# Performance work log

Hardware: AMD Instinct MI355X
Metric: run time of the kernel (lower is better)

The kernel has to match this reference:

```python
import jax, jax.numpy as jnp
import numpy as np

B, L, C, W, NH, FS = 8, 8, 64, 32, 128, 5
PAD = FS // 2
LN_EPS = 1e-5


def _conv(x, w, b, pad):
    y = jax.lax.conv_general_dilated(x, w, (1, 1), [(pad, pad), (pad, pad)],
                                     dimension_numbers=('NCHW', 'OIHW', 'NCHW'))
    return y + b[None, :, None, None]


def _stem(x, w1, b1, lnw, lnb, w2, b2):
    # conv(fs) -> LayerNorm over [C,W,W] -> ReLU -> conv(1x1)
    y = _conv(x, w1, b1, PAD)
    mu = jnp.mean(y, axis=(1, 2, 3), keepdims=True)
    var = jnp.var(y, axis=(1, 2, 3), keepdims=True)
    y = (y - mu) * jax.lax.rsqrt(var + LN_EPS) * lnw[None] + lnb[None]
    return _conv(jax.nn.relu(y), w2, b2, 0)


def setup_inputs() -> dict:
    key = jax.random.key(0)
    ks = jax.random.split(key, 8)
    f = lambda k, shp: jax.random.normal(k, shp, jnp.float32) * 0.02
    return {
        'in_query': jax.random.normal(ks[0], (B, C, W, W), jnp.float32),
        'in_keys': jax.random.normal(ks[1], (B, L, C, W, W), jnp.float32),
        'in_values': jax.random.normal(ks[2], (B, L, C, W, W), jnp.float32),
        's_w1': f(ks[3], (C, C, FS, FS)), 's_b1': jnp.zeros((C,), jnp.float32),
        's_lnw': jnp.ones((C, W, W), jnp.float32), 's_lnb': jnp.zeros((C, W, W), jnp.float32),
        's_w2': f(ks[4], (NH, C, 1, 1)), 's_b2': jnp.zeros((NH,), jnp.float32),
        'c_w1': f(ks[5], (C, C, FS, FS)), 'c_b1': jnp.zeros((C,), jnp.float32),
        'c_lnw': jnp.ones((C, W, W), jnp.float32), 'c_lnb': jnp.zeros((C, W, W), jnp.float32),
        'c_w2': f(ks[6], (NH, C, 1, 1)), 'c_b2': jnp.zeros((NH,), jnp.float32),
    }


def reference(in_query, in_keys, in_values,
              s_w1, s_b1, s_lnw, s_lnb, s_w2, s_b2,
              c_w1, c_b1, c_lnw, c_lnb, c_w2, c_b2):
    b, c, w, h = in_query.shape
    l = in_keys.shape[1]
    # ---- spatial attention: tokens = pixels, features = channels ----
    qf = in_query.reshape(b, c, w * h).transpose(0, 2, 1)            # [B, WH, C]
    kf = in_keys.transpose(0, 1, 3, 4, 2).reshape(b, l * w * h, c)   # [B, LWH, C]
    vf = in_values.transpose(0, 1, 3, 4, 2).reshape(b, l * w * h, c)
    a_sp = jax.nn.softmax(jnp.einsum('bnc,bmc->bnm', qf, kf), axis=-1)  # [B, WH, LWH]
    sp = jnp.einsum('bnm,bmc->bnc', a_sp, vf).reshape(b, w, h, c).transpose(0, 3, 1, 2)
    # ---- channel attention: tokens = channels, features = pixels ----
    qc = in_query.reshape(b, c, w * h)                               # [B, C, WH]
    kc = in_keys.reshape(b, l * c, h * w)                            # [B, LC, WH]
    vc = in_values.reshape(b, l * c, h * w)
    a_ch = jax.nn.softmax(jnp.einsum('bcn,bmn->bcm', qc, kc), axis=-1)  # [B, C, LC]
    ch = jnp.einsum('bcm,bmn->bcn', a_ch, vc).reshape(b, c, w, h)
    # ---- conv-LN-ReLU-conv stems on residual-added branches ----
    s_attn = _stem(sp + in_query, s_w1, s_b1, s_lnw, s_lnb, s_w2, s_b2)
    c_attn = _stem(ch + in_query, c_w1, c_b1, c_lnw, c_lnb, c_w2, c_b2)
    return (s_attn, c_attn)
```

## Files before the change

kernel.cpp:

```cpp
#include <hip/hip_runtime.h>


#define LOG2E 1.44269504088896340736f

typedef __attribute__((ext_vector_type(8))) short short8;
typedef __attribute__((ext_vector_type(4))) float f4;

#define MFMA16(a, b, c) __builtin_amdgcn_mfma_f32_16x16x32_bf16(a, b, c, 0, 0, 0)

#define GLOAD_LDS16(gp, lp) __builtin_amdgcn_global_load_lds( \
    (const __attribute__((address_space(1))) void*)(gp), \
    (__attribute__((address_space(3))) void*)(lp), 16, 0, 0)

__device__ __forceinline__ unsigned short f2bf(float f) {
  union { float f; unsigned u; } v; v.f = f;
  unsigned r = v.u + 0x7FFFu + ((v.u >> 16) & 1u);
  return (unsigned short)(r >> 16);
}
__device__ __forceinline__ unsigned short f2bf_rz(float f) {
  union { float f; unsigned u; } v; v.f = f;
  return (unsigned short)(v.u >> 16);
}
__device__ __forceinline__ float bf2f(unsigned short h) {
  union { unsigned u; float f; } v; v.u = ((unsigned)h) << 16;
  return v.f;
}
__device__ __forceinline__ float exp2fast(float x) {
#if __has_builtin(__builtin_amdgcn_exp2f)
  return __builtin_amdgcn_exp2f(x);
#else
  return exp2f(x);
#endif
}

#define O_STATS 0ul
#define O_W1T   256ul
#define O_W2B   409856ul
#define O_LNW   442624ul
#define O_LNB   704768ul
#define O_QT    966912ul
#define O_KSP   2015488ul
#define O_VT    10404096ul
#define O_NUM   18792704ul
#define O_DEN   35569920ul
#define O_SP    36094208ul
#define O_PCH   40288512ul
#define O_XS    40812800ul
#define O_XC    41861376ul
#define O_YT    42909952ul

__global__ __launch_bounds__(256) void k1_prep_chanS(
    const float* __restrict__ q, const float* __restrict__ keys,
    const float* __restrict__ values,
    const float* __restrict__ sw1, const float* __restrict__ slnw,
    const float* __restrict__ slnb, const float* __restrict__ sw2,
    const float* __restrict__ cw1, const float* __restrict__ clnw,
    const float* __restrict__ clnb, const float* __restrict__ cw2,
    char* __restrict__ ws)
{
  __shared__ float T[64][65];
  const int job = blockIdx.x, t = threadIdx.x;

  if (job < 2240) {
    int kind, mat = 0, sel = 0;
    if (job < 1024)      { kind = 0; mat = job >> 4; }
    else if (job < 2048) { kind = 1; mat = (job - 1024) >> 4; }
    else if (job < 2176) { kind = 2; mat = (job - 2048) >> 4; }
    else                 { kind = 3; sel = (job - 2176) >> 4; }
    const int pt = job & 15, p0 = pt * 64;
    const float* src =
        kind == 0 ? keys : kind == 1 ? values : kind == 2 ? q
        : (sel == 0 ? slnw : sel == 1 ? slnb : sel == 2 ? clnw : clnb);
    src += (size_t)mat * 65536;

    const int r0 = t >> 4, c4 = (t & 15) * 4;
    if (kind == 1) {
      unsigned short* VTp = (unsigned short*)(ws + O_VT);
      const int b = mat >> 3, l = mat & 7;
#pragma unroll
      for (int pass = 0; pass < 4; ++pass) {
        const int r = pass * 16 + r0;
        float4 v = *(const float4*)(src + (size_t)r * 1024 + p0 + c4);
        ushort4 o;
        o.x = f2bf(v.x); o.y = f2bf(v.y); o.z = f2bf(v.z); o.w = f2bf(v.w);
        *(ushort4*)(VTp + ((size_t)b * 64 + r) * 8192 + l * 1024 + p0 + c4) = o;
      }
      return;
    }
#pragma unroll
    for (int pass = 0; pass < 4; ++pass) {
      const int r = pass * 16 + r0;
      float4 v = *(const float4*)(src + (size_t)r * 1024 + p0 + c4);
      T[r][c4] = v.x; T[r][c4 + 1] = v.y; T[r][c4 + 2] = v.z; T[r][c4 + 3] = v.w;
    }
    __syncthreads();
#pragma unroll
    for (int pass = 0; pass < 2; ++pass) {
      const int p = pass * 32 + (t >> 3), cs = (t & 7) * 8;
      short8 o;
      if (kind == 0) {
#pragma unroll
        for (int j = 0; j < 8; ++j) o[j] = (short)f2bf(T[cs + j][p] * LOG2E);
        const int b = mat >> 3, l = mat & 7;
        *(short8*)((unsigned short*)(ws + O_KSP) +
                   ((size_t)b * 8192 + l * 1024 + p0 + p) * 64 + cs) = o;
      } else if (kind == 2) {
#pragma unroll
        for (int j = 0; j < 8; ++j) o[j] = (short)f2bf(T[cs + j][p]);
        *(short8*)((unsigned short*)(ws + O_QT) +
                   ((size_t)mat * 1024 + p0 + p) * 64 + cs) = o;
      } else {
#pragma unroll
        for (int j = 0; j < 8; ++j) o[j] = (short)f2bf(T[cs + j][p]);
        unsigned long off = (sel & 1) ? O_LNB : O_LNW;
        *(short8*)((unsigned short*)(ws + off) +
                   ((size_t)(sel >> 1) * 1024 + p0 + p) * 64 + cs) = o;
      }
    }
    return;
  }

  if (job < 3104) {
    unsigned i = (job - 2240) * 256u + t;
    if (i < 204800u) {
      unsigned ci = i & 63u, co = (i >> 6) & 63u, tt = i >> 12;
      unsigned off = tt % 25u, st = tt / 25u;
      const float* w = st ? cw1 : sw1;
      ((unsigned short*)(ws + O_W1T))[i] = f2bf(w[(co * 64u + ci) * 25u + off]);
      return;
    }
    i -= 204800u;
    if (i < 16384u) {
      unsigned c = i & 63u, nh = (i >> 6) & 127u, st = i >> 13;
      const float* w = st ? cw2 : sw2;
      ((unsigned short*)(ws + O_W2B))[i] = f2bf(w[nh * 64u + c]);
    }
    return;
  }

  {
    float* Sp = (float*)(ws + O_SP);
    const int bid = job - 3104;
    const int b = bid >> 5, colT = (bid >> 2) & 7, kt = bid & 3;
    const int w = t >> 6, lane = t & 63;
    const int low4 = lane & 15, quad = lane >> 4;
    const int col0 = colT * 64 + w * 16;

    f4 acc[4];
#pragma unroll
    for (int m = 0; m < 4; ++m) acc[m] = (f4){0.f, 0.f, 0.f, 0.f};

#pragma unroll
    for (int kst = 0; kst < 8; ++kst) {
      const int k = kt * 256 + kst * 32 + quad * 8;
      const float* kp = keys + ((size_t)(b * 512 + col0 + low4)) * 1024 + k;
      float4 u0 = *(const float4*)kp;
      float4 u1 = *(const float4*)(kp + 4);
      float kv[8] = {u0.x, u0.y, u0.z, u0.w, u1.x, u1.y, u1.z, u1.w};
      short8 bh, bl;
#pragma unroll
      for (int j = 0; j < 8; ++j) {
        unsigned short hi = f2bf(kv[j]);
        bh[j] = (short)hi;
        bl[j] = (short)f2bf(kv[j] - bf2f(hi));
      }
#pragma unroll
      for (int m = 0; m < 4; ++m) {
        const float* qp = q + ((size_t)(b * 64 + m * 16 + low4)) * 1024 + k;
        float4 w0 = *(const float4*)qp;
        float4 w1 = *(const float4*)(qp + 4);
        float qv[8] = {w0.x, w0.y, w0.z, w0.w, w1.x, w1.y, w1.z, w1.w};
        short8 ah, al;
#pragma unroll
        for (int j = 0; j < 8; ++j) {
          float sv = qv[j] * LOG2E;
          unsigned short hi = f2bf(sv);
          ah[j] = (short)hi;
          al[j] = (short)f2bf(sv - bf2f(hi));
        }
        acc[m] = MFMA16(ah, bh, acc[m]);
        acc[m] = MFMA16(al, bh, acc[m]);
        acc[m] = MFMA16(ah, bl, acc[m]);
      }
    }
#pragma unroll
    for (int m = 0; m < 4; ++m)
#pragma unroll
      for (int r = 0; r < 4; ++r)
        Sp[(((size_t)kt * 8 + b) * 64 + m * 16 + quad * 4 + r) * 512 + col0 + low4] = acc[m][r];
  }
}

__global__ __launch_bounds__(256, 2) void k2_spat_soft(char* __restrict__ ws)
{
  __shared__ __align__(16) unsigned short Kt[2][4096];
  __shared__ __align__(16) unsigned short Vt[2][4096];
  __shared__ __align__(16) unsigned short Pl[4][4096];

  if (blockIdx.x < 512) {
    const unsigned short* QT = (const unsigned short*)(ws + O_QT);
    const unsigned short* KSP = (const unsigned short*)(ws + O_KSP);
    const unsigned short* VTg = (const unsigned short*)(ws + O_VT);
    unsigned short* NUM = (unsigned short*)(ws + O_NUM);
    float* DEN = (float*)(ws + O_DEN);

    const int b = blockIdx.x >> 6;
    const int qt = (blockIdx.x >> 4) & 3;
    const int s = blockIdx.x & 15;
    const int t = threadIdx.x;
    const int w = t >> 6, lane = t & 63;
    const int low4 = lane & 15, quad = lane >> 4;

    const unsigned short* KSPb = KSP + (size_t)b * 8192 * 64;
    const unsigned short* VTb = VTg + (size_t)b * 64 * 8192;
    const int qbase = qt * 256 + w * 64;
    const int kvbase = s * 512;

    int cn[2], cks[2], cqd[2], cl4[2];
#pragma unroll
    for (int pass = 0; pass < 2; ++pass) {
      const int c = pass * 256 + t;
      cn[pass] = c >> 7; cks[pass] = (c >> 6) & 1;
      cqd[pass] = (c >> 4) & 3; cl4[pass] = c & 15;
    }

    short8 qa[4][2];
#pragma unroll
    for (int mi = 0; mi < 4; ++mi)
#pragma unroll
      for (int ks = 0; ks < 2; ++ks)
        qa[mi][ks] = *(const short8*)(QT +
            ((size_t)(b * 1024 + qbase + mi * 16 + low4)) * 64 + ks * 32 + quad * 8);

    short8 vones;
#pragma unroll
    for (int j = 0; j < 8; ++j) vones[j] = (short)0x3F80;

    f4 accO[4][4], accD[4];
#pragma unroll
    for (int m = 0; m < 4; ++m) {
      accD[m] = (f4){0.f, 0.f, 0.f, 0.f};
#pragma unroll
      for (int n = 0; n < 4; ++n) accO[m][n] = (f4){0.f, 0.f, 0.f, 0.f};
    }

#pragma unroll
    for (int pass = 0; pass < 2; ++pass) {
      const int kv0 = kvbase;
      GLOAD_LDS16(KSPb + ((size_t)(kv0 + cn[pass] * 16 + cl4[pass])) * 64 +
                      cks[pass] * 32 + cqd[pass] * 8,
                  &Kt[0][(pass * 256 + w * 64) * 8]);
      GLOAD_LDS16(VTb + ((size_t)(cn[pass] * 16 + cl4[pass])) * 8192 + kv0 +
                      cks[pass] * 32 + cqd[pass] * 8,
                  &Vt[0][(pass * 256 + w * 64) * 8]);
    }

    const int pswz = ((low4 >> 2) & 3) << 1;
    for (int it = 0; it < 8; ++it) {
      const int d = it & 1;
      __syncthreads();
      if (it < 7) {
        const int kv1 = kvbase + (it + 1) * 64;
#pragma unroll
        for (int pass = 0; pass < 2; ++pass) {
          GLOAD_LDS16(KSPb + ((size_t)(kv1 + cn[pass] * 16 + cl4[pass])) * 64 +
                          cks[pass] * 32 + cqd[pass] * 8,
                      &Kt[d ^ 1][(pass * 256 + w * 64) * 8]);
          GLOAD_LDS16(VTb + ((size_t)(cn[pass] * 16 + cl4[pass])) * 8192 + kv1 +
                          cks[pass] * 32 + cqd[pass] * 8,
                      &Vt[d ^ 1][(pass * 256 + w * 64) * 8]);
        }
      }
#pragma unroll
      for (int n = 0; n < 4; ++n) {
        f4 sS[4];
#pragma unroll
        for (int mi = 0; mi < 4; ++mi) sS[mi] = (f4){0.f, 0.f, 0.f, 0.f};
#pragma unroll
        for (int ks = 0; ks < 2; ++ks) {
          short8 kb = *(const short8*)&Kt[d][((n * 2 + ks) * 64 + lane) * 8];
#pragma unroll
          for (int mi = 0; mi < 4; ++mi) sS[mi] = MFMA16(qa[mi][ks], kb, sS[mi]);
        }
        const int cpr = (((n * 2 + (low4 >> 3)) ^ (quad << 1)) << 3) + (low4 & 7);
#pragma unroll
        for (int mi = 0; mi < 4; ++mi) {
          unsigned short* pw = &Pl[w][(mi * 16 + quad * 4) * 64 + cpr];
#pragma unroll
          for (int r = 0; r < 4; ++r)
            pw[r * 64] = f2bf_rz(exp2fast(sS[mi][r]));
        }
      }
#pragma unroll
      for (int ks = 0; ks < 2; ++ks) {
        short8 vb[4];
#pragma unroll
        for (int n2 = 0; n2 < 4; ++n2)
          vb[n2] = *(const short8*)&Vt[d][((n2 * 2 + ks) * 64 + lane) * 8];
        const int cr = (((ks * 4 + quad) ^ pswz) << 3);
#pragma unroll
        for (int m = 0; m < 4; ++m) {
          short8 pa = *(const short8*)&Pl[w][(m * 16 + low4) * 64 + cr];
          accD[m] = MFMA16(pa, vones, accD[m]);
#pragma unroll
          for (int n2 = 0; n2 < 4; ++n2) accO[m][n2] = MFMA16(pa, vb[n2], accO[m][n2]);
        }
      }
    }

#pragma unroll
    for (int m = 0; m < 4; ++m)
#pragma unroll
      for (int r = 0; r < 4; ++r) {
        const int row = qbase + m * 16 + quad * 4 + r;
        const size_t base = ((size_t)(b * 1024 + row) * 16 + s);
#pragma unroll
        for (int n2 = 0; n2 < 4; ++n2)
          NUM[base * 64 + n2 * 16 + low4] = f2bf(accO[m][n2][r]);
        if (low4 == 0) DEN[base] = accD[m][r];
      }
    return;
  }

  {
    const float* Sp = (const float*)(ws + O_SP);
    unsigned short* P = (unsigned short*)(ws + O_PCH);
    const int bid = blockIdx.x - 512;
    const int b = bid >> 2, rt = bid & 3;
    const int row = rt * 16 + (threadIdx.x >> 4), tc = threadIdx.x & 15;

    float sv[32];
    float mx = -1e30f;
#pragma unroll
    for (int jj = 0; jj < 32; ++jj) {
      const int col = jj * 16 + tc;
      size_t base = ((size_t)b * 64 + row) * 512 + col;
      float v = Sp[base] + Sp[base + 262144] + Sp[base + 524288] + Sp[base + 786432];
      sv[jj] = v;
      mx = fmaxf(mx, v);
    }
#pragma unroll
    for (int o = 1; o < 16; o <<= 1) mx = fmaxf(mx, __shfl_xor(mx, o, 64));
    float sum = 0.f;
#pragma unroll
    for (int jj = 0; jj < 32; ++jj) {
      float e = exp2fast(sv[jj] - mx);
      sv[jj] = e;
      sum += e;
    }
#pragma unroll
    for (int o = 1; o < 16; o <<= 1) sum += __shfl_xor(sum, o, 64);
    const float rs = 1.0f / sum;
#pragma unroll
    for (int jj = 0; jj < 32; ++jj)
      P[((size_t)b * 64 + row) * 512 + jj * 16 + tc] = f2bf(sv[jj] * rs);
  }
}

__global__ __launch_bounds__(256) void k3_fin_chanB(const float* __restrict__ values,
                                                    char* __restrict__ ws)
{
  const unsigned short* QT = (const unsigned short*)(ws + O_QT);

  if (blockIdx.x < 512) {
    const unsigned short* NUM = (const unsigned short*)(ws + O_NUM);
    const float* DEN = (const float*)(ws + O_DEN);
    unsigned short* Xs = (unsigned short*)(ws + O_XS);

    const unsigned i = blockIdx.x * 256u + threadIdx.x;
    const int c0 = (i & 15) * 4;
    const unsigned row = i >> 4;

    float dtot = 0.f;
#pragma unroll
    for (int sq = 0; sq < 4; ++sq) {
      float4 dv = *(const float4*)(DEN + (size_t)row * 16 + sq * 4);
      dtot += dv.x + dv.y + dv.z + dv.w;
    }
    float n4[4] = {0.f, 0.f, 0.f, 0.f};
#pragma unroll
    for (int s = 0; s < 16; ++s) {
      ushort4 pv = *(const ushort4*)(NUM + ((size_t)row * 16 + s) * 64 + c0);
      n4[0] += bf2f(pv.x); n4[1] += bf2f(pv.y);
      n4[2] += bf2f(pv.z); n4[3] += bf2f(pv.w);
    }
    const float rd = 1.0f / dtot;
    size_t ob = (size_t)row * 64 + c0;
    ushort4 qv = *(const ushort4*)(QT + ob);
    ushort4 o4;
    o4.x = f2bf(n4[0] * rd + bf2f(qv.x));
    o4.y = f2bf(n4[1] * rd + bf2f(qv.y));
    o4.z = f2bf(n4[2] * rd + bf2f(qv.z));
    o4.w = f2bf(n4[3] * rd + bf2f(qv.w));
    *(ushort4*)(Xs + ob) = o4;
    return;
  }

  {
    const unsigned short* P = (const unsigned short*)(ws + O_PCH);
    unsigned short* Xc = (unsigned short*)(ws + O_XC);

    const int bid = blockIdx.x - 512;
    const int b = bid >> 4, pt = bid & 15;
    const int w = threadIdx.x >> 6, lane = threadIdx.x & 63;
    const int low4 = lane & 15, quad = lane >> 4;
    const int p = pt * 64 + w * 16 + low4;

    f4 acc[4];
#pragma unroll
    for (int m = 0; m < 4; ++m) acc[m] = (f4){0.f, 0.f, 0.f, 0.f};

    const float* vbase = values + (size_t)b * 524288 + p;
    for (int ks = 0; ks < 16; ++ks) {
      short8 vbv;
      const float* vp = vbase + (size_t)(ks * 32 + quad * 8) * 1024;
#pragma unroll
      for (int j = 0; j < 8; ++j) vbv[j] = (short)f2bf(vp[(size_t)j * 1024]);
#pragma unroll
      for (int m = 0; m < 4; ++m) {
        short8 a = *(const short8*)(P + ((size_t)(b * 64 + m * 16 + low4)) * 512 + ks * 32 + quad * 8);
        acc[m] = MFMA16(a, vbv, acc[m]);
      }
    }
#pragma unroll
    for (int m = 0; m < 4; ++m)
#pragma unroll
      for (int r = 0; r < 4; ++r) {
        const int c = m * 16 + quad * 4 + r;
        size_t o = ((size_t)(b * 1024 + p)) * 64 + c;
        Xc[o] = f2bf(acc[m][r] + bf2f(QT[o]));
      }
  }
}

__global__ __launch_bounds__(512) void k4_conv5(char* __restrict__ ws,
                                                const float* __restrict__ sb1,
                                                const float* __restrict__ cb1)
{
  const int id = blockIdx.x;
  const int s = id >> 8, b = (id >> 5) & 7, pt = id & 31;
  const int t = threadIdx.x;
  const int w = t >> 6, lane = t & 63;
  const int low4 = lane & 15, quad = lane >> 4;
  const int wsub = w & 1, quarter = w >> 1;

  const unsigned short* X = (const unsigned short*)(ws + (s ? O_XC : O_XS));
  const unsigned short* W1t = (const unsigned short*)(ws + O_W1T);
  unsigned short* Yt = (unsigned short*)(ws + O_YT);
  float* stats = (float*)(ws + O_STATS);
  const float* b1p = s ? cb1 : sb1;

  __shared__ float Hbuf[3][2][16][65];
  __shared__ float red[2][2];

  const int p = pt * 32 + wsub * 16 + low4;
  const int y0 = p >> 5, x0 = p & 31;

  f4 acc[4];
#pragma unroll
  for (int m = 0; m < 4; ++m) acc[m] = (f4){0.f, 0.f, 0.f, 0.f};

  const int o0 = quarter == 0 ? 0 : quarter == 1 ? 7 : quarter == 2 ? 13 : 19;
  const int o1 = quarter == 0 ? 7 : quarter == 1 ? 13 : quarter == 2 ? 19 : 25;
  for (int off = o0; off < o1; ++off) {
    const int dy = off / 5 - 2, dx = off % 5 - 2;
    const int ys = y0 + dy, xs = x0 + dx;
    const bool valid = ((unsigned)ys < 32u) & ((unsigned)xs < 32u);
    const int psrc = valid ? (p + dy * 32 + dx) : p;
    const unsigned short* xp = X + ((size_t)(b * 1024 + psrc)) * 64;
    const unsigned short* wp = W1t + ((size_t)((s * 25 + off) * 64)) * 64;
#pragma unroll
    for (int ks = 0; ks < 2; ++ks) {
      short8 bv = *(const short8*)(xp + ks * 32 + quad * 8);
      if (!valid) bv = (short8)0;
#pragma unroll
      for (int m = 0; m < 4; ++m) {
        short8 av = *(const short8*)(wp + (m * 16 + low4) * 64 + ks * 32 + quad * 8);
        acc[m] = MFMA16(av, bv, acc[m]);
      }
    }
  }

  if (quarter) {
#pragma unroll
    for (int m = 0; m < 4; ++m)
#pragma unroll
      for (int r = 0; r < 4; ++r)
        Hbuf[quarter - 1][wsub][low4][m * 16 + quad * 4 + r] = acc[m][r];
  }
  __syncthreads();
  if (!quarter) {
    float ls = 0.f, ls2 = 0.f;
#pragma unroll
    for (int m = 0; m < 4; ++m)
#pragma unroll
      for (int r = 0; r < 4; ++r) {
        const int co = m * 16 + quad * 4 + r;
        float y = acc[m][r] + Hbuf[0][wsub][low4][co] + Hbuf[1][wsub][low4][co] +
                  Hbuf[2][wsub][low4][co] + b1p[co];
        Yt[((size_t)((s * 8 + b) * 1024 + p)) * 64 + co] = f2bf(y);
        ls += y; ls2 += y * y;
      }
#pragma unroll
    for (int o = 1; o < 64; o <<= 1) {
      ls += __shfl_xor(ls, o, 64);
      ls2 += __shfl_xor(ls2, o, 64);
    }
    if (lane == 0) { red[0][wsub] = ls; red[1][wsub] = ls2; }
  }
  __syncthreads();
  if (t == 0) {
    atomicAdd(&stats[(s * 8 + b) * 2 + 0], red[0][0] + red[0][1]);
    atomicAdd(&stats[(s * 8 + b) * 2 + 1], red[1][0] + red[1][1]);
  }
}

__global__ __launch_bounds__(256) void k5_final(char* __restrict__ ws,
                                                const float* __restrict__ sb2,
                                                const float* __restrict__ cb2,
                                                float* __restrict__ out)
{
  const int id = blockIdx.x;
  const int s = id >> 8, b = (id >> 5) & 7, pt = id & 31;
  const int w = threadIdx.x >> 6, lane = threadIdx.x & 63;
  const int low4 = lane & 15, quad = lane >> 4;
  const int p2 = pt * 32 + (w & 1) * 16 + low4;
  const int nh0 = (w >> 1) * 64;

  const unsigned short* Yt = (const unsigned short*)(ws + O_YT);
  const unsigned short* LNW = (const unsigned short*)(ws + O_LNW);
  const unsigned short* LNB = (const unsigned short*)(ws + O_LNB);
  const unsigned short* W2b = (const unsigned short*)(ws + O_W2B);
  const float* stats = (const float*)(ws + O_STATS);
  const float* b2p = s ? cb2 : sb2;

  const float inv = 1.0f / 65536.0f;
  const float mu = stats[(s * 8 + b) * 2 + 0] * inv;
  const float ms = stats[(s * 8 + b) * 2 + 1] * inv;
  const float rsig = rsqrtf(ms - mu * mu + 1e-5f);

  f4 acc[4];
#pragma unroll
  for (int m = 0; m < 4; ++m) acc[m] = (f4){0.f, 0.f, 0.f, 0.f};

#pragma unroll
  for (int ks = 0; ks < 2; ++ks) {
    size_t yo = ((size_t)((s * 8 + b) * 1024 + p2)) * 64 + ks * 32 + quad * 8;
    size_t lo = ((size_t)(s * 1024 + p2)) * 64 + ks * 32 + quad * 8;
    short8 yv = *(const short8*)(Yt + yo);
    short8 lw8 = *(const short8*)(LNW + lo);
    short8 lb8 = *(const short8*)(LNB + lo);
    short8 zv;
#pragma unroll
    for (int j = 0; j < 8; ++j) {
      float z = (bf2f((unsigned short)yv[j]) - mu) * rsig * bf2f((unsigned short)lw8[j]) +
                bf2f((unsigned short)lb8[j]);
      zv[j] = (short)f2bf(fmaxf(z, 0.f));
    }
#pragma unroll
    for (int m = 0; m < 4; ++m) {
      short8 a = *(const short8*)(W2b + ((size_t)(s * 128 + nh0 + m * 16 + low4)) * 64 + ks * 32 + quad * 8);
      acc[m] = MFMA16(a, zv, acc[m]);
    }
  }
#pragma unroll
  for (int m = 0; m < 4; ++m)
#pragma unroll
    for (int r = 0; r < 4; ++r) {
      const int nh = nh0 + m * 16 + quad * 4 + r;
      out[((size_t)((s * 8 + b) * 128 + nh)) * 1024 + p2] = acc[m][r] + b2p[nh];
    }
}

extern "C" void kernel_launch(void* const* d_in, const int* in_sizes, int n_in,
                              void* d_out, int out_size, void* d_ws, size_t ws_size,
                              hipStream_t stream)
{
  const float* q    = (const float*)d_in[0];
  const float* keys = (const float*)d_in[1];
  const float* vals = (const float*)d_in[2];
  const float* sw1  = (const float*)d_in[3];
  const float* sb1  = (const float*)d_in[4];
  const float* slnw = (const float*)d_in[5];
  const float* slnb = (const float*)d_in[6];
  const float* sw2  = (const float*)d_in[7];
  const float* sb2  = (const float*)d_in[8];
  const float* cw1  = (const float*)d_in[9];
  const float* cb1  = (const float*)d_in[10];
  const float* clnw = (const float*)d_in[11];
  const float* clnb = (const float*)d_in[12];
  const float* cw2  = (const float*)d_in[13];
  const float* cb2  = (const float*)d_in[14];
  char* ws = (char*)d_ws;

  hipMemsetAsync(ws + O_STATS, 0, 256, stream);
  k1_prep_chanS<<<3360, 256, 0, stream>>>(q, keys, vals, sw1, slnw, slnb, sw2,
                                          cw1, clnw, clnb, cw2, ws);
  k2_spat_soft<<<544, 256, 0, stream>>>(ws);
  k3_fin_chanB<<<640, 256, 0, stream>>>(vals, ws);
  k4_conv5<<<512, 512, 0, stream>>>(ws, sb1, cb1);
  k5_final<<<512, 256, 0, stream>>>(ws, sb2, cb2, (float*)d_out);
}
```

Before: 232.2 us.

## Reschedule kernel stages to co-run independent branches and stage channel scores via LDS

Moves the channel-attention score GEMM from the prep kernel into the spatial-attention kernel. It now stages q and keys tiles through LDS with double-buffered direct global-to-LDS loads, each wave covering two column tiles. The channel softmax moves into the finalize kernel. The channel PV GEMM is paired with the spatial conv, and the channel conv with the spatial final 1x1, so independent stages share launches. The 5x5 conv now uses 256-thread blocks with two K-halves instead of four, which means more serial work per wave and one more kernel launch.

```diff
diff --git a/kernel.cpp b/kernel.cpp
--- a/kernel.cpp
+++ b/kernel.cpp
@@ -49,7 +49,7 @@
 #define O_XC    41861376ul
 #define O_YT    42909952ul
 
-__global__ __launch_bounds__(256) void k1_prep_chanS(
+__global__ __launch_bounds__(256) void k1_prep(
     const float* __restrict__ q, const float* __restrict__ keys,
     const float* __restrict__ values,
     const float* __restrict__ sw1, const float* __restrict__ slnw,
@@ -120,7 +120,7 @@
     return;
   }
 
-  if (job < 3104) {
+  {
     unsigned i = (job - 2240) * 256u + t;
     if (i < 204800u) {
       unsigned ci = i & 63u, co = (i >> 6) & 63u, tt = i >> 12;
@@ -135,69 +135,20 @@
       const float* w = st ? cw2 : sw2;
       ((unsigned short*)(ws + O_W2B))[i] = f2bf(w[nh * 64u + c]);
     }
-    return;
-  }
-
-  {
-    float* Sp = (float*)(ws + O_SP);
-    const int bid = job - 3104;
-    const int b = bid >> 5, colT = (bid >> 2) & 7, kt = bid & 3;
-    const int w = t >> 6, lane = t & 63;
-    const int low4 = lane & 15, quad = lane >> 4;
-    const int col0 = colT * 64 + w * 16;
-
-    f4 acc[4];
-#pragma unroll
-    for (int m = 0; m < 4; ++m) acc[m] = (f4){0.f, 0.f, 0.f, 0.f};
-
-#pragma unroll
-    for (int kst = 0; kst < 8; ++kst) {
-      const int k = kt * 256 + kst * 32 + quad * 8;
-      const float* kp = keys + ((size_t)(b * 512 + col0 + low4)) * 1024 + k;
-      float4 u0 = *(const float4*)kp;
-      float4 u1 = *(const float4*)(kp + 4);
-      float kv[8] = {u0.x, u0.y, u0.z, u0.w, u1.x, u1.y, u1.z, u1.w};
-      short8 bh, bl;
-#pragma unroll
-      for (int j = 0; j < 8; ++j) {
-        unsigned short hi = f2bf(kv[j]);
-        bh[j] = (short)hi;
-        bl[j] = (short)f2bf(kv[j] - bf2f(hi));
-      }
-#pragma unroll
-      for (int m = 0; m < 4; ++m) {
-        const float* qp = q + ((size_t)(b * 64 + m * 16 + low4)) * 1024 + k;
-        float4 w0 = *(const float4*)qp;
-        float4 w1 = *(const float4*)(qp + 4);
-        float qv[8] = {w0.x, w0.y, w0.z, w0.w, w1.x, w1.y, w1.z, w1.w};
-        short8 ah, al;
-#pragma unroll
-        for (int j = 0; j < 8; ++j) {
-          float sv = qv[j] * LOG2E;
-          unsigned short hi = f2bf(sv);
-          ah[j] = (short)hi;
-          al[j] = (short)f2bf(sv - bf2f(hi));
-        }
-        acc[m] = MFMA16(ah, bh, acc[m]);
-        acc[m] = MFMA16(al, bh, acc[m]);
-        acc[m] = MFMA16(ah, bl, acc[m]);
-      }
-    }
-#pragma unroll
-    for (int m = 0; m < 4; ++m)
-#pragma unroll
-      for (int r = 0; r < 4; ++r)
-        Sp[(((size_t)kt * 8 + b) * 64 + m * 16 + quad * 4 + r) * 512 + col0 + low4] = acc[m][r];
-  }
-}
-
-__global__ __launch_bounds__(256, 2) void k2_spat_soft(char* __restrict__ ws)
-{
-  __shared__ __align__(16) unsigned short Kt[2][4096];
-  __shared__ __align__(16) unsigned short Vt[2][4096];
-  __shared__ __align__(16) unsigned short Pl[4][4096];
+  }
+}
+
+__global__ __launch_bounds__(256) void k2_spat_chanS(
+    const float* __restrict__ q, const float* __restrict__ keys,
+    char* __restrict__ ws)
+{
+  __shared__ __align__(16) unsigned char SM[65536];
 
   if (blockIdx.x < 512) {
+    unsigned short (*Kt)[4096] = (unsigned short(*)[4096])(SM);
+    unsigned short (*Vt)[4096] = (unsigned short(*)[4096])(SM + 16384);
+    unsigned short (*Pl)[4096] = (unsigned short(*)[4096])(SM + 32768);
+
     const unsigned short* QT = (const unsigned short*)(ws + O_QT);
     const unsigned short* KSP = (const unsigned short*)(ws + O_KSP);
     const unsigned short* VTg = (const unsigned short*)(ws + O_VT);
@@ -246,11 +197,10 @@
 
 #pragma unroll
     for (int pass = 0; pass < 2; ++pass) {
-      const int kv0 = kvbase;
-      GLOAD_LDS16(KSPb + ((size_t)(kv0 + cn[pass] * 16 + cl4[pass])) * 64 +
+      GLOAD_LDS16(KSPb + ((size_t)(kvbase + cn[pass] * 16 + cl4[pass])) * 64 +
                       cks[pass] * 32 + cqd[pass] * 8,
                   &Kt[0][(pass * 256 + w * 64) * 8]);
-      GLOAD_LDS16(VTb + ((size_t)(cn[pass] * 16 + cl4[pass])) * 8192 + kv0 +
+      GLOAD_LDS16(VTb + ((size_t)(cn[pass] * 16 + cl4[pass])) * 8192 + kvbase +
                       cks[pass] * 32 + cqd[pass] * 8,
                   &Vt[0][(pass * 256 + w * 64) * 8]);
     }
@@ -323,48 +273,105 @@
   }
 
   {
-    const float* Sp = (const float*)(ws + O_SP);
-    unsigned short* P = (unsigned short*)(ws + O_PCH);
+    float* Sp = (float*)(ws + O_SP);
     const int bid = blockIdx.x - 512;
-    const int b = bid >> 2, rt = bid & 3;
-    const int row = rt * 16 + (threadIdx.x >> 4), tc = threadIdx.x & 15;
-
-    float sv[32];
-    float mx = -1e30f;
-#pragma unroll
-    for (int jj = 0; jj < 32; ++jj) {
-      const int col = jj * 16 + tc;
-      size_t base = ((size_t)b * 64 + row) * 512 + col;
-      float v = Sp[base] + Sp[base + 262144] + Sp[base + 524288] + Sp[base + 786432];
-      sv[jj] = v;
-      mx = fmaxf(mx, v);
-    }
-#pragma unroll
-    for (int o = 1; o < 16; o <<= 1) mx = fmaxf(mx, __shfl_xor(mx, o, 64));
-    float sum = 0.f;
-#pragma unroll
-    for (int jj = 0; jj < 32; ++jj) {
-      float e = exp2fast(sv[jj] - mx);
-      sv[jj] = e;
-      sum += e;
-    }
-#pragma unroll
-    for (int o = 1; o < 16; o <<= 1) sum += __shfl_xor(sum, o, 64);
-    const float rs = 1.0f / sum;
-#pragma unroll
-    for (int jj = 0; jj < 32; ++jj)
-      P[((size_t)b * 64 + row) * 512 + jj * 16 + tc] = f2bf(sv[jj] * rs);
-  }
-}
-
-__global__ __launch_bounds__(256) void k3_fin_chanB(const float* __restrict__ values,
-                                                    char* __restrict__ ws)
-{
-  const unsigned short* QT = (const unsigned short*)(ws + O_QT);
-
+    const int b = bid >> 4, colT = (bid >> 2) & 3, kt = bid & 3;
+    const int t = threadIdx.x, w = t >> 6, lane = t & 63;
+    const int low4 = lane & 15, quad = lane >> 4;
+    const int dl = lane >> 1, dh = lane & 1;
+    const int k00 = kt * 256;
+
+    f4 acc[4][2];
+#pragma unroll
+    for (int m = 0; m < 4; ++m)
+#pragma unroll
+      for (int n = 0; n < 2; ++n) acc[m][n] = (f4){0.f, 0.f, 0.f, 0.f};
+
+    auto stageAll = [&](int bo, int k0) {
+#pragma unroll
+      for (int gi = 0; gi < 4; ++gi) {
+        const int g = w + gi * 4;
+        const int n = g >> 1, sub = g & 1;
+        const int l = sub * 32 + dl;
+        const float* gp = keys + (size_t)(b * 512 + colT * 128 + n * 16 + (l & 15)) * 1024
+                          + k0 + (l >> 4) * 8 + dh * 4;
+        GLOAD_LDS16(gp, SM + bo + (size_t)(n * 128 + sub * 64) * 16);
+      }
+#pragma unroll
+      for (int gi = 0; gi < 2; ++gi) {
+        const int g = w + gi * 4;
+        const int m = g >> 1, sub = g & 1;
+        const int l = sub * 32 + dl;
+        const float* gp = q + (size_t)(b * 64 + m * 16 + (l & 15)) * 1024
+                          + k0 + (l >> 4) * 8 + dh * 4;
+        GLOAD_LDS16(gp, SM + bo + 16384 + (size_t)(m * 128 + sub * 64) * 16);
+      }
+    };
+
+    stageAll(0, k00);
+    for (int it = 0; it < 8; ++it) {
+      const int bo = (it & 1) * 24576;
+      const char* cb = (const char*)SM + bo;
+      __syncthreads();
+      if (it < 7) stageAll(bo ^ 24576, k00 + (it + 1) * 32);
+
+      short8 ah[4], al[4];
+#pragma unroll
+      for (int m = 0; m < 4; ++m) {
+        const float* fp = (const float*)(cb + 16384 + (size_t)(m * 128 + lane * 2) * 16);
+        float4 u0 = ((const float4*)fp)[0];
+        float4 u1 = ((const float4*)fp)[1];
+        float vv[8] = {u0.x, u0.y, u0.z, u0.w, u1.x, u1.y, u1.z, u1.w};
+#pragma unroll
+        for (int j = 0; j < 8; ++j) {
+          float sv = vv[j] * LOG2E;
+          unsigned short hi = f2bf(sv);
+          ah[m][j] = (short)hi;
+          al[m][j] = (short)f2bf(sv - bf2f(hi));
+        }
+      }
+#pragma unroll
+      for (int n2 = 0; n2 < 2; ++n2) {
+        const int n = w * 2 + n2;
+        const float* fp = (const float*)(cb + (size_t)(n * 128 + lane * 2) * 16);
+        float4 u0 = ((const float4*)fp)[0];
+        float4 u1 = ((const float4*)fp)[1];
+        float vv[8] = {u0.x, u0.y, u0.z, u0.w, u1.x, u1.y, u1.z, u1.w};
+        short8 bh, bl;
+#pragma unroll
+        for (int j = 0; j < 8; ++j) {
+          unsigned short hi = f2bf(vv[j]);
+          bh[j] = (short)hi;
+          bl[j] = (short)f2bf(vv[j] - bf2f(hi));
+        }
+#pragma unroll
+        for (int m = 0; m < 4; ++m) {
+          acc[m][n2] = MFMA16(ah[m], bh, acc[m][n2]);
+          acc[m][n2] = MFMA16(al[m], bh, acc[m][n2]);
+          acc[m][n2] = MFMA16(ah[m], bl, acc[m][n2]);
+        }
+      }
+    }
+
+#pragma unroll
+    for (int m = 0; m < 4; ++m)
+#pragma unroll
+      for (int n2 = 0; n2 < 2; ++n2)
+#pragma unroll
+        for (int r = 0; r < 4; ++r) {
+          const int row = m * 16 + quad * 4 + r;
+          const int col = colT * 128 + (w * 2 + n2) * 16 + low4;
+          Sp[(((size_t)kt * 8 + b) * 64 + row) * 512 + col] = acc[m][n2][r];
+        }
+  }
+}
+
+__global__ __launch_bounds__(256) void k3_fin_soft(char* __restrict__ ws)
+{
   if (blockIdx.x < 512) {
     const unsigned short* NUM = (const unsigned short*)(ws + O_NUM);
     const float* DEN = (const float*)(ws + O_DEN);
+    const unsigned short* QT = (const unsigned short*)(ws + O_QT);
     unsigned short* Xs = (unsigned short*)(ws + O_XS);
 
     const unsigned i = blockIdx.x * 256u + threadIdx.x;
@@ -397,61 +404,54 @@
   }
 
   {
-    const unsigned short* P = (const unsigned short*)(ws + O_PCH);
-    unsigned short* Xc = (unsigned short*)(ws + O_XC);
-
+    const float* Sp = (const float*)(ws + O_SP);
+    unsigned short* P = (unsigned short*)(ws + O_PCH);
     const int bid = blockIdx.x - 512;
-    const int b = bid >> 4, pt = bid & 15;
-    const int w = threadIdx.x >> 6, lane = threadIdx.x & 63;
-    const int low4 = lane & 15, quad = lane >> 4;
-    const int p = pt * 64 + w * 16 + low4;
-
-    f4 acc[4];
-#pragma unroll
-    for (int m = 0; m < 4; ++m) acc[m] = (f4){0.f, 0.f, 0.f, 0.f};
-
-    const float* vbase = values + (size_t)b * 524288 + p;
-    for (int ks = 0; ks < 16; ++ks) {
-      short8 vbv;
-      const float* vp = vbase + (size_t)(ks * 32 + quad * 8) * 1024;
-#pragma unroll
-      for (int j = 0; j < 8; ++j) vbv[j] = (short)f2bf(vp[(size_t)j * 1024]);
-#pragma unroll
-      for (int m = 0; m < 4; ++m) {
-        short8 a = *(const short8*)(P + ((size_t)(b * 64 + m * 16 + low4)) * 512 + ks * 32 + quad * 8);
-        acc[m] = MFMA16(a, vbv, acc[m]);
-      }
-    }
-#pragma unroll
-    for (int m = 0; m < 4; ++m)
-#pragma unroll
-      for (int r = 0; r < 4; ++r) {
-        const int c = m * 16 + quad * 4 + r;
-        size_t o = ((size_t)(b * 1024 + p)) * 64 + c;
-        Xc[o] = f2bf(acc[m][r] + bf2f(QT[o]));
-      }
-  }
-}
-
-__global__ __launch_bounds__(512) void k4_conv5(char* __restrict__ ws,
-                                                const float* __restrict__ sb1,
-                                                const float* __restrict__ cb1)
-{
-  const int id = blockIdx.x;
-  const int s = id >> 8, b = (id >> 5) & 7, pt = id & 31;
-  const int t = threadIdx.x;
-  const int w = t >> 6, lane = t & 63;
+    const int b = bid >> 2, rt = bid & 3;
+    const int row = rt * 16 + (threadIdx.x >> 4), tc = threadIdx.x & 15;
+
+    float sv[32];
+    float mx = -1e30f;
+#pragma unroll
+    for (int jj = 0; jj < 32; ++jj) {
+      const int col = jj * 16 + tc;
+      size_t base = ((size_t)b * 64 + row) * 512 + col;
+      float v = Sp[base] + Sp[base + 262144] + Sp[base + 524288] + Sp[base + 786432];
+      sv[jj] = v;
+      mx = fmaxf(mx, v);
+    }
+#pragma unroll
+    for (int o = 1; o < 16; o <<= 1) mx = fmaxf(mx, __shfl_xor(mx, o, 64));
+    float sum = 0.f;
+#pragma unroll
+    for (int jj = 0; jj < 32; ++jj) {
+      float e = exp2fast(sv[jj] - mx);
+      sv[jj] = e;
+      sum += e;
+    }
+#pragma unroll
+    for (int o = 1; o < 16; o <<= 1) sum += __shfl_xor(sum, o, 64);
+    const float rs = 1.0f / sum;
+#pragma unroll
+    for (int jj = 0; jj < 32; ++jj)
+      P[((size_t)b * 64 + row) * 512 + jj * 16 + tc] = f2bf(sv[jj] * rs);
+  }
+}
+
+__device__ __forceinline__ void conv5_body(char* ws, const float* b1p, int s, int bid)
+{
+  __shared__ float Hbuf[2][16][65];
+  __shared__ float red[2][2];
+
+  const int b = bid >> 5, pt = bid & 31;
+  const int w = threadIdx.x >> 6, lane = threadIdx.x & 63;
   const int low4 = lane & 15, quad = lane >> 4;
-  const int wsub = w & 1, quarter = w >> 1;
+  const int wsub = w & 1, half = w >> 1;
 
   const unsigned short* X = (const unsigned short*)(ws + (s ? O_XC : O_XS));
   const unsigned short* W1t = (const unsigned short*)(ws + O_W1T);
   unsigned short* Yt = (unsigned short*)(ws + O_YT);
   float* stats = (float*)(ws + O_STATS);
-  const float* b1p = s ? cb1 : sb1;
-
-  __shared__ float Hbuf[3][2][16][65];
-  __shared__ float red[2][2];
 
   const int p = pt * 32 + wsub * 16 + low4;
   const int y0 = p >> 5, x0 = p & 31;
@@ -460,8 +460,7 @@
 #pragma unroll
   for (int m = 0; m < 4; ++m) acc[m] = (f4){0.f, 0.f, 0.f, 0.f};
 
-  const int o0 = quarter == 0 ? 0 : quarter == 1 ? 7 : quarter == 2 ? 13 : 19;
-  const int o1 = quarter == 0 ? 7 : quarter == 1 ? 13 : quarter == 2 ? 19 : 25;
+  const int o0 = half ? 13 : 0, o1 = half ? 25 : 13;
   for (int off = o0; off < o1; ++off) {
     const int dy = off / 5 - 2, dx = off % 5 - 2;
     const int ys = y0 + dy, xs = x0 + dx;
@@ -481,23 +480,22 @@
     }
   }
 
-  if (quarter) {
+  if (half) {
 #pragma unroll
     for (int m = 0; m < 4; ++m)
 #pragma unroll
       for (int r = 0; r < 4; ++r)
-        Hbuf[quarter - 1][wsub][low4][m * 16 + quad * 4 + r] = acc[m][r];
+        Hbuf[wsub][low4][m * 16 + quad * 4 + r] = acc[m][r];
   }
   __syncthreads();
-  if (!quarter) {
+  if (!half) {
     float ls = 0.f, ls2 = 0.f;
 #pragma unroll
     for (int m = 0; m < 4; ++m)
 #pragma unroll
       for (int r = 0; r < 4; ++r) {
         const int co = m * 16 + quad * 4 + r;
-        float y = acc[m][r] + Hbuf[0][wsub][low4][co] + Hbuf[1][wsub][low4][co] +
-                  Hbuf[2][wsub][low4][co] + b1p[co];
+        float y = acc[m][r] + Hbuf[wsub][low4][co] + b1p[co];
         Yt[((size_t)((s * 8 + b) * 1024 + p)) * 64 + co] = f2bf(y);
         ls += y; ls2 += y * y;
       }
@@ -509,19 +507,16 @@
     if (lane == 0) { red[0][wsub] = ls; red[1][wsub] = ls2; }
   }
   __syncthreads();
-  if (t == 0) {
+  if (threadIdx.x == 0) {
     atomicAdd(&stats[(s * 8 + b) * 2 + 0], red[0][0] + red[0][1]);
     atomicAdd(&stats[(s * 8 + b) * 2 + 1], red[1][0] + red[1][1]);
   }
 }
 
-__global__ __launch_bounds__(256) void k5_final(char* __restrict__ ws,
-                                                const float* __restrict__ sb2,
-                                                const float* __restrict__ cb2,
-                                                float* __restrict__ out)
-{
-  const int id = blockIdx.x;
-  const int s = id >> 8, b = (id >> 5) & 7, pt = id & 31;
+__device__ __forceinline__ void final_body(char* ws, const float* b2p,
+                                           float* out, int s, int bid)
+{
+  const int b = bid >> 5, pt = bid & 31;
   const int w = threadIdx.x >> 6, lane = threadIdx.x & 63;
   const int low4 = lane & 15, quad = lane >> 4;
   const int p2 = pt * 32 + (w & 1) * 16 + low4;
@@ -532,7 +527,6 @@
   const unsigned short* LNB = (const unsigned short*)(ws + O_LNB);
   const unsigned short* W2b = (const unsigned short*)(ws + O_W2B);
   const float* stats = (const float*)(ws + O_STATS);
-  const float* b2p = s ? cb2 : sb2;
 
   const float inv = 1.0f / 65536.0f;
   const float mu = stats[(s * 8 + b) * 2 + 0] * inv;
@@ -570,6 +564,63 @@
       const int nh = nh0 + m * 16 + quad * 4 + r;
       out[((size_t)((s * 8 + b) * 128 + nh)) * 1024 + p2] = acc[m][r] + b2p[nh];
     }
+}
+
+__global__ __launch_bounds__(256) void k4_conv5s_chanB(
+    const float* __restrict__ values, char* __restrict__ ws,
+    const float* __restrict__ sb1)
+{
+  if (blockIdx.x < 256) { conv5_body(ws, sb1, 0, blockIdx.x); return; }
+
+  const unsigned short* P = (const unsigned short*)(ws + O_PCH);
+  const unsigned short* QT = (const unsigned short*)(ws + O_QT);
+  unsigned short* Xc = (unsigned short*)(ws + O_XC);
+
+  const int bid = blockIdx.x - 256;
+  const int b = bid >> 4, pt = bid & 15;
+  const int w = threadIdx.x >> 6, lane = threadIdx.x & 63;
+  const int low4 = lane & 15, quad = lane >> 4;
+  const int p = pt * 64 + w * 16 + low4;
+
+  f4 acc[4];
+#pragma unroll
+  for (int m = 0; m < 4; ++m) acc[m] = (f4){0.f, 0.f, 0.f, 0.f};
+
+  const float* vbase = values + (size_t)b * 524288 + p;
+  for (int ks = 0; ks < 16; ++ks) {
+    short8 vbv;
+    const float* vp = vbase + (size_t)(ks * 32 + quad * 8) * 1024;
+#pragma unroll
+    for (int j = 0; j < 8; ++j) vbv[j] = (short)f2bf(vp[(size_t)j * 1024]);
+#pragma unroll
+    for (int m = 0; m < 4; ++m) {
+      short8 a = *(const short8*)(P + ((size_t)(b * 64 + m * 16 + low4)) * 512 + ks * 32 + quad * 8);
+      acc[m] = MFMA16(a, vbv, acc[m]);
+    }
+  }
+#pragma unroll
+  for (int m = 0; m < 4; ++m)
+#pragma unroll
+    for (int r = 0; r < 4; ++r) {
+      const int c = m * 16 + quad * 4 + r;
+      size_t o = ((size_t)(b * 1024 + p)) * 64 + c;
+      Xc[o] = f2bf(acc[m][r] + bf2f(QT[o]));
+    }
+}
+
+__global__ __launch_bounds__(256) void k5_conv5c_finS(
+    char* __restrict__ ws, const float* __restrict__ cb1,
+    const float* __restrict__ sb2, float* __restrict__ out)
+{
+  if (blockIdx.x < 256) { conv5_body(ws, cb1, 1, blockIdx.x); return; }
+  final_body(ws, sb2, out, 0, blockIdx.x - 256);
+}
+
+__global__ __launch_bounds__(256) void k6_finC(
+    char* __restrict__ ws, const float* __restrict__ cb2,
+    float* __restrict__ out)
+{
+  final_body(ws, cb2, out, 1, blockIdx.x);
 }
 
 extern "C" void kernel_launch(void* const* d_in, const int* in_sizes, int n_in,
@@ -593,11 +644,12 @@
   const float* cb2  = (const float*)d_in[14];
   char* ws = (char*)d_ws;
 
-  hipMemsetAsync(ws + O_STATS, 0, 256, stream);
-  k1_prep_chanS<<<3360, 256, 0, stream>>>(q, keys, vals, sw1, slnw, slnb, sw2,
-                                          cw1, clnw, clnb, cw2, ws);
-  k2_spat_soft<<<544, 256, 0, stream>>>(ws);
-  k3_fin_chanB<<<640, 256, 0, stream>>>(vals, ws);
-  k4_conv5<<<512, 512, 0, stream>>>(ws, sb1, cb1);
-  k5_final<<<512, 256, 0, stream>>>(ws, sb2, cb2, (float*)d_out);
-}
+  (void)hipMemsetAsync(ws + O_STATS, 0, 256, stream);
+  k1_prep<<<3104, 256, 0, stream>>>(q, keys, vals, sw1, slnw, slnb, sw2,
+                                    cw1, clnw, clnb, cw2, ws);
+  k2_spat_chanS<<<640, 256, 0, stream>>>(q, keys, ws);
+  k3_fin_soft<<<544, 256, 0, stream>>>(ws);
+  k4_conv5s_chanB<<<384, 256, 0, stream>>>(vals, ws, sb1);
+  k5_conv5c_finS<<<512, 256, 0, stream>>>(ws, cb1, sb2, (float*)d_out);
+  k6_finC<<<256, 256, 0, stream>>>(ws, cb2, (float*)d_out);
+}
```

After: 211.4 us. 1.1x faster.
